# Optimization experiments

Measured on AMD Instinct MI355X. Metric: run time of the kernel, lower is better.

Reference implementation:

```python
import jax, jax.numpy as jnp
import numpy as np
import math
from itertools import combinations_with_replacement

# --- static config matching init_kwargs ---
L = 64          # input_lenght
ORDER = 2       # polynomial order
DIV = 100       # weight_divisor
B = 16384       # batch size

# Precomputed index tuples for combinations-with-replacement of the L inputs.
# Shape: (n_comb, ORDER) with n_comb = C(L+ORDER-1, ORDER) = 2080 for L=64, r=2.
IDX = np.array(list(combinations_with_replacement(range(L), ORDER)), dtype=np.int32)
# Number of weights includes the bias slot: C(L+1+ORDER-1, ORDER) = 2145.
# The original _get_colx only fills the first n_comb columns; the rest stay zero.
NUM_W = math.comb(L + 1 + ORDER - 1, ORDER)


def setup_inputs() -> dict:
    key = jax.random.key(0)
    k1, k2, k3 = jax.random.split(key, 3)
    x = jax.random.normal(k1, (B, L), dtype=jnp.float32)
    W = jax.random.uniform(k2, (NUM_W,), dtype=jnp.float32) / DIV
    b = jax.random.uniform(k3, (1,), dtype=jnp.float32) / DIV
    return {"x": x, "W": W, "b": b}


def reference(x, W, b):
    idx = jnp.asarray(IDX)                      # (n_comb, ORDER)
    # gather + product: colx[i, p] = prod_j x[i, idx[p, j]]
    colx = jnp.prod(x[:, idx], axis=-1)         # (B, n_comb)
    pad = NUM_W - colx.shape[1]                 # trailing zero columns (bias-slot artifact)
    colx = jnp.pad(colx, ((0, 0), (0, pad)))    # (B, NUM_W)
    out = colx @ W.reshape(-1, 1) + b           # (B, 1)
    return out
```

## Files before the change

kernel.cpp:

```cpp
#include <hip/hip_runtime.h>


#define ROWS 64
#define XSTRIDE 65

__global__ __launch_bounds__(1024, 4) void honu_kernel(
    const float* __restrict__ X, const float* __restrict__ W,
    const float* __restrict__ Bias, float* __restrict__ out, int nrows) {
  __shared__ float tile[ROWS * XSTRIDE];
  __shared__ float part[16][64];

  const int tid = threadIdx.x;
  const int lane = tid & 63;
  const int row0 = blockIdx.x * ROWS;

  {
    const int r = tid >> 4;
    const int c = (tid & 15) << 2;
    float4 v = make_float4(0.f, 0.f, 0.f, 0.f);
    if (row0 + r < nrows) {
      v = reinterpret_cast<const float4*>(X)[(size_t)(row0 + r) * 16 +
                                             (tid & 15)];
    }
    float* dst = &tile[r * XSTRIDE + c];
    dst[0] = v.x;
    dst[1] = v.y;
    dst[2] = v.z;
    dst[3] = v.w;
  }
  __syncthreads();

  const float* xrow = &tile[lane * XSTRIDE];

  float x[64];
#pragma unroll
  for (int k = 0; k < 64; ++k) x[k] = xrow[k];

  const int s = __builtin_amdgcn_readfirstlane(tid >> 6);

  float acc = 0.0f;
#pragma unroll
  for (int jj = 0; jj < 4; ++jj) {
    const int j = 4 * s + jj;
    const int base2 = 63 * j - (j * (j - 1)) / 2;
    float y = 0.0f;
#pragma unroll
    for (int k = 0; k < 64; ++k) {
      const float wv = W[base2 + k];
      const float w = (k >= j) ? wv : 0.0f;
      y = __builtin_fmaf(w, x[k], y);
    }
    acc = __builtin_fmaf(xrow[j], y, acc);
  }

  part[tid >> 6][lane] = acc;
  __syncthreads();

  if (tid < 64) {
    const int orow = row0 + tid;
    if (orow < nrows) {
      float r = Bias[0];
#pragma unroll
      for (int w = 0; w < 16; ++w) r += part[w][tid];
      out[orow] = r;
    }
  }
}

extern "C" void kernel_launch(void* const* d_in, const int* in_sizes, int n_in,
                              void* d_out, int out_size, void* d_ws,
                              size_t ws_size, hipStream_t stream) {
  const float* X = (const float*)d_in[0];
  const float* W = (const float*)d_in[1];
  const float* Bias = (const float*)d_in[2];
  float* out = (float*)d_out;

  const int nrows = out_size;
  const int grid = (nrows + ROWS - 1) / ROWS;
  honu_kernel<<<grid, 1024, 0, stream>>>(X, W, Bias, out, nrows);
}
```

Measured before the change: 63.00 us.

## Map one row per wavefront with readlane broadcast and shuffle reduction

```diff
diff --git a/kernel.cpp b/kernel.cpp
--- a/kernel.cpp
+++ b/kernel.cpp
@@ -1,70 +1,35 @@
 #include <hip/hip_runtime.h>
 
 
-#define ROWS 64
-#define XSTRIDE 65
+#define WAVES_PER_BLOCK 8
+#define BLOCK (WAVES_PER_BLOCK * 64)
 
-__global__ __launch_bounds__(1024, 4) void honu_kernel(
+__global__ __launch_bounds__(BLOCK) void honu_kernel(
     const float* __restrict__ X, const float* __restrict__ W,
     const float* __restrict__ Bias, float* __restrict__ out, int nrows) {
-  __shared__ float tile[ROWS * XSTRIDE];
-  __shared__ float part[16][64];
+  const int lane = threadIdx.x & 63;
+  const int wave = threadIdx.x >> 6;
+  const int row = blockIdx.x * WAVES_PER_BLOCK + wave;
+  if (row >= nrows) return;
 
-  const int tid = threadIdx.x;
-  const int lane = tid & 63;
-  const int row0 = blockIdx.x * ROWS;
+  const float xv = X[(size_t)row * 64 + lane];
 
-  {
-    const int r = tid >> 4;
-    const int c = (tid & 15) << 2;
-    float4 v = make_float4(0.f, 0.f, 0.f, 0.f);
-    if (row0 + r < nrows) {
-      v = reinterpret_cast<const float4*>(X)[(size_t)(row0 + r) * 16 +
-                                             (tid & 15)];
-    }
-    float* dst = &tile[r * XSTRIDE + c];
-    dst[0] = v.x;
-    dst[1] = v.y;
-    dst[2] = v.z;
-    dst[3] = v.w;
-  }
-  __syncthreads();
-
-  const float* xrow = &tile[lane * XSTRIDE];
-
-  float x[64];
+  float z = 0.0f;
 #pragma unroll
-  for (int k = 0; k < 64; ++k) x[k] = xrow[k];
-
-  const int s = __builtin_amdgcn_readfirstlane(tid >> 6);
-
-  float acc = 0.0f;
-#pragma unroll
-  for (int jj = 0; jj < 4; ++jj) {
-    const int j = 4 * s + jj;
-    const int base2 = 63 * j - (j * (j - 1)) / 2;
-    float y = 0.0f;
-#pragma unroll
-    for (int k = 0; k < 64; ++k) {
-      const float wv = W[base2 + k];
-      const float w = (k >= j) ? wv : 0.0f;
-      y = __builtin_fmaf(w, x[k], y);
-    }
-    acc = __builtin_fmaf(xrow[j], y, acc);
+  for (int j = 0; j < 64; ++j) {
+    const int cj = 63 * j - (j * (j - 1)) / 2;
+    float w = W[cj + lane];
+    w = (lane >= j) ? w : 0.0f;
+    const float xj = __int_as_float(
+        __builtin_amdgcn_readlane(__float_as_int(xv), j));
+    z = __builtin_fmaf(w, xj, z);
   }
 
-  part[tid >> 6][lane] = acc;
-  __syncthreads();
+  float p = xv * z;
+#pragma unroll
+  for (int off = 32; off > 0; off >>= 1) p += __shfl_xor(p, off);
 
-  if (tid < 64) {
-    const int orow = row0 + tid;
-    if (orow < nrows) {
-      float r = Bias[0];
-#pragma unroll
-      for (int w = 0; w < 16; ++w) r += part[w][tid];
-      out[orow] = r;
-    }
-  }
+  if (lane == 0) out[row] = p + Bias[0];
 }
 
 extern "C" void kernel_launch(void* const* d_in, const int* in_sizes, int n_in,
@@ -76,6 +41,6 @@
   float* out = (float*)d_out;
 
   const int nrows = out_size;
-  const int grid = (nrows + ROWS - 1) / ROWS;
-  honu_kernel<<<grid, 1024, 0, stream>>>(X, W, Bias, out, nrows);
+  const int grid = (nrows + WAVES_PER_BLOCK - 1) / WAVES_PER_BLOCK;
+  honu_kernel<<<grid, BLOCK, 0, stream>>>(X, W, Bias, out, nrows);
 }
```

After: 66.93 us. +6.2%, slower.
